# Performance work log

Measured on AMD Instinct MI355X. Metric: run time of the kernel, lower is better.

The kernel has to match this reference:

```python
import jax, jax.numpy as jnp
import numpy as np

N = 100000   # nodes
E = 1600000  # edges
G = 256      # graphs in batch
F_IN = 64
H = 64
C = 10


def setup_inputs() -> dict:
    key = jax.random.key(0)
    ks = jax.random.split(key, 16)
    x = jax.random.normal(ks[0], (N, F_IN), dtype=jnp.float32)
    edge_index = jax.random.randint(ks[1], (2, E), 0, N, dtype=jnp.int32)
    batch = jnp.sort(jax.random.randint(ks[2], (N,), 0, G, dtype=jnp.int32))
    def lin(k, i, o):
        return jax.random.normal(k, (i, o), dtype=jnp.float32) / np.sqrt(i).astype(np.float32)
    return {
        'x': x, 'edge_index': edge_index, 'batch': batch,
        'W1': lin(ks[3], F_IN, H), 'b1': jnp.zeros((H,), jnp.float32),
        'W2': lin(ks[4], H, H),    'b2': jnp.zeros((H,), jnp.float32),
        'W3': lin(ks[5], H, H),    'b3': jnp.zeros((H,), jnp.float32),
        'fc1_w': lin(ks[6], 3 * H, H),      'fc1_b': jnp.zeros((H,), jnp.float32),
        'fc2_w': lin(ks[7], H, H // 2),     'fc2_b': jnp.zeros((H // 2,), jnp.float32),
        'fc3_w': lin(ks[8], H // 2, C),     'fc3_b': jnp.zeros((C,), jnp.float32),
    }


def _gcn_layer(h_in, W, b, src, dst, deg_inv_sqrt):
    # GCNConv: h = X W ; out = D^-1/2 (A + I) D^-1/2 h + b ; then ReLU
    h = h_in @ W
    norm = deg_inv_sqrt[src] * deg_inv_sqrt[dst]            # [E]
    agg = jax.ops.segment_sum(h[src] * norm[:, None], dst, num_segments=N)
    agg = agg + h * (deg_inv_sqrt * deg_inv_sqrt)[:, None]  # self-loop term
    return jax.nn.relu(agg + b)


def _pool(h, batch):
    # concat(mean, max, add) pooling by graph id
    s = jax.ops.segment_sum(h, batch, num_segments=G)
    cnt = jax.ops.segment_sum(jnp.ones((h.shape[0], 1), h.dtype), batch, num_segments=G)
    mean = s / jnp.maximum(cnt, 1.0)
    mx = jnp.maximum(jax.ops.segment_max(h, batch, num_segments=G), 0.0)  # h >= 0 post-ReLU
    return jnp.concatenate([mean, mx, s], axis=1)  # [G, 3H]


def reference(x, edge_index, batch, W1, b1, W2, b2, W3, b3,
              fc1_w, fc1_b, fc2_w, fc2_b, fc3_w, fc3_b):
    src, dst = edge_index[0], edge_index[1]
    # degree including self loop (edge weight 1)
    deg = jax.ops.segment_sum(jnp.ones((E,), x.dtype), dst, num_segments=N) + 1.0
    dis = jax.lax.rsqrt(deg)

    h1 = _gcn_layer(x, W1, b1, src, dst, dis)
    p1 = _pool(h1, batch)
    h2 = _gcn_layer(h1, W2, b2, src, dst, dis)
    p2 = _pool(h2, batch)
    h3 = _gcn_layer(h2, W3, b3, src, dst, dis)
    p3 = _pool(h3, batch)

    z = p1 + p2 + p3                              # [G, 3H]
    z = jax.nn.relu(z @ fc1_w + fc1_b)            # dropout inactive (eval)
    z = jax.nn.relu(z @ fc2_w + fc2_b)
    return jax.nn.log_softmax(z @ fc3_w + fc3_b, axis=-1)
```

## Files before the change

### kernel.cpp

```cpp
#include <hip/hip_runtime.h>
#include <cmath>

typedef unsigned int uint;
typedef __attribute__((ext_vector_type(8))) short short8;
typedef __attribute__((ext_vector_type(4))) float f32x4;
typedef __attribute__((ext_vector_type(4))) int i32x4;

__device__ inline float bflo(uint u) { return __uint_as_float(u << 16); }
__device__ inline float bfhi(uint u) { return __uint_as_float(u & 0xffff0000u); }
__device__ inline ushort bf1(float a) {
  uint ua = __float_as_uint(a);
  return (ushort)((ua + 0x7fffu + ((ua >> 16) & 1u)) >> 16);
}
__device__ inline uint bfpack(float a, float b) {
  uint ua = __float_as_uint(a), ub = __float_as_uint(b);
  uint ra = (ua + 0x7fffu + ((ua >> 16) & 1u)) >> 16;
  uint rb = (ub + 0x7fffu + ((ub >> 16) & 1u)) >> 16;
  return ra | (rb << 16);
}

#define SLOT_CAP 48
#define FILL_CHUNK 4096
#define BSHIFT 8
#define NPB 256
#define MAXB 512
#define BCAP 5120
#define PSPLIT 4

__global__ __launch_bounds__(256) void part_k(const int* __restrict__ src, const int* __restrict__ dst,
                                              int* __restrict__ bcnt, long long* __restrict__ buckets,
                                              int E, int nb) {
  __shared__ int lcnt[MAXB], lbase[MAXB];
  int t = threadIdx.x;
  for (int i = t; i < nb; i += 256) lcnt[i] = 0;
  __syncthreads();
  int base = blockIdx.x * FILL_CHUNK;
  int d[16];
  #pragma unroll
  for (int i = 0; i < 16; ++i) {
    int e = base + t + i * 256;
    d[i] = (e < E) ? __builtin_nontemporal_load(dst + e) : -1;
    if (d[i] >= 0) atomicAdd(&lcnt[d[i] >> BSHIFT], 1);
  }
  __syncthreads();
  for (int i = t; i < nb; i += 256) { lbase[i] = atomicAdd(&bcnt[i], lcnt[i]); lcnt[i] = 0; }
  __syncthreads();
  #pragma unroll
  for (int i = 0; i < 16; ++i) {
    if (d[i] >= 0) {
      int e = base + t + i * 256;
      int r = d[i] >> BSHIFT;
      int rank = atomicAdd(&lcnt[r], 1);
      long long s = (long long)__builtin_nontemporal_load(src + e);
      long long packed = (s << 32) | (unsigned int)d[i];
      buckets[(size_t)r * BCAP + lbase[r] + rank] = packed;
    }
  }
}

__global__ __launch_bounds__(256) void fillB_k(const long long* __restrict__ buckets,
                                               const int* __restrict__ bcnt,
                                               int* __restrict__ cursor, int* __restrict__ csr,
                                               float* __restrict__ dis,
                                               int nb, int N) {
  __shared__ int lcnt[NPB];
  __shared__ int rows[NPB][SLOT_CAP];
  int r = blockIdx.x;
  int t = threadIdx.x;
  if (t < NPB) lcnt[t] = 0;
  i32x4* rinit = (i32x4*)&rows[0][0];
  for (int i = t; i < NPB * SLOT_CAP / 4; i += 256) rinit[i] = (i32x4){N, N, N, N};
  __syncthreads();
  int n = bcnt[r];
  const long long* bk = buckets + (size_t)r * BCAP;
  for (int i = t; i < n; i += 256) {
    long long e = __builtin_nontemporal_load(&bk[i]);
    int dl = (int)(e & (NPB - 1));
    int s = (int)(e >> 32);
    int pos = atomicAdd(&lcnt[dl], 1);
    if (pos < SLOT_CAP) rows[dl][pos] = s;
  }
  __syncthreads();
  int base_node = r << BSHIFT;
  int nodes_here = N - base_node; if (nodes_here > NPB) nodes_here = NPB;
  if (nodes_here <= 0) return;
  int total4 = nodes_here * (SLOT_CAP / 4);
  i32x4* dstp = (i32x4*)(csr + (size_t)base_node * SLOT_CAP);
  const i32x4* srcp = (const i32x4*)&rows[0][0];
  for (int i = t; i < total4; i += 256) dstp[i] = srcp[i];
  for (int i = t; i < nodes_here; i += 256) {
    int c = lcnt[i];
    cursor[base_node + i] = c;
    dis[base_node + i] = rsqrtf((float)c + 1.0f);
  }
}

__global__ __launch_bounds__(256) void bounds_k(const int* __restrict__ batch, int* __restrict__ gstart,
                                                int n, int G) {
  int i = blockIdx.x * 256 + threadIdx.x;
  if (i >= n) return;
  int b = batch[i];
  int prev = (i == 0) ? -1 : batch[i - 1];
  for (int g = prev + 1; g <= b; ++g) gstart[g] = i;
  if (i == n - 1) { for (int g = b + 1; g <= G; ++g) gstart[g] = n; }
}

__global__ __launch_bounds__(256) void xcast_k(const float* __restrict__ X, ushort* __restrict__ Y, int total4) {
  int i = blockIdx.x * 256 + threadIdx.x;
  if (i >= total4) return;
  float4 v = ((const float4*)X)[i];
  ((uint2*)Y)[i] = make_uint2(bfpack(v.x, v.y), bfpack(v.z, v.w));
}

__global__ __launch_bounds__(256) void wt3_k(const float* __restrict__ W1, const float* __restrict__ W2,
                                             const float* __restrict__ W3,
                                             ushort* __restrict__ T1, ushort* __restrict__ T2,
                                             ushort* __restrict__ T3) {
  int b = blockIdx.x >> 4;
  int i = (blockIdx.x & 15) * 256 + threadIdx.x;
  const float* W = (b == 0) ? W1 : (b == 1) ? W2 : W3;
  ushort* T = (b == 0) ? T1 : (b == 1) ? T2 : T3;
  int c = i >> 6, k = i & 63;
  T[i] = bf1(W[k * 64 + c]);
}

__global__ __launch_bounds__(256) void gemm_mfma_k(const ushort* __restrict__ X,
                                                   const ushort* __restrict__ WT,
                                                   const float* __restrict__ dis,
                                                   ushort* __restrict__ Y, int n) {
  int t = threadIdx.x;
  int wv = t >> 6, lane = t & 63;
  int m = lane & 15, quad = lane >> 4;
  int row = blockIdx.x * 64 + wv * 16 + m;
  int rclamp = (row < n) ? row : 0;
  const short8* arow = (const short8*)(X + (size_t)rclamp * 64);
  short8 a0 = arow[quad];
  short8 a1 = arow[quad + 4];
  f32x4 acc[4];
  #pragma unroll
  for (int ct = 0; ct < 4; ++ct) {
    const short8* wrow = (const short8*)(WT + (size_t)(ct * 16 + m) * 64);
    short8 b0 = wrow[quad];
    short8 b1 = wrow[quad + 4];
    f32x4 a = {0.f, 0.f, 0.f, 0.f};
    a = __builtin_amdgcn_mfma_f32_16x16x32_bf16(a0, b0, a, 0, 0, 0);
    a = __builtin_amdgcn_mfma_f32_16x16x32_bf16(a1, b1, a, 0, 0, 0);
    acc[ct] = a;
  }
  int orow = blockIdx.x * 64 + wv * 16 + quad * 4;
  #pragma unroll
  for (int reg = 0; reg < 4; ++reg) {
    int r = orow + reg;
    if (r < n) {
      float ds = dis[r];
      #pragma unroll
      for (int ct = 0; ct < 4; ++ct)
        Y[(size_t)r * 64 + ct * 16 + m] = bf1(acc[ct][reg] * ds);
    }
  }
}

__global__ __launch_bounds__(256) void agg_k(const ushort* __restrict__ Hs,
                                             const int* __restrict__ csr,
                                             const int* __restrict__ cnt,
                                             const float* __restrict__ dis,
                                             const float* __restrict__ bias,
                                             ushort* __restrict__ Hout, int n) {
  int wv = __builtin_amdgcn_readfirstlane((int)(threadIdx.x >> 6));
  int lane = threadIdx.x & 63;
  int node = blockIdx.x * 4 + wv;
  if (node >= n) return;
  float dn = dis[node];
  int deg = __builtin_nontemporal_load(cnt + node);
  if (deg > SLOT_CAP) deg = SLOT_CAP;
  const i32x4* rp = (const i32x4*)(csr + (size_t)node * SLOT_CAP);
  float acc = bflo((uint)Hs[(size_t)node * 64 + lane]);

  i32x4 r0 = __builtin_nontemporal_load(rp + 0);
  i32x4 r1 = __builtin_nontemporal_load(rp + 1);
  i32x4 r2 = __builtin_nontemporal_load(rp + 2);
  i32x4 r3 = __builtin_nontemporal_load(rp + 3);
  i32x4 r4 = __builtin_nontemporal_load(rp + 4);
  i32x4 r5 = __builtin_nontemporal_load(rp + 5);
  i32x4 r6 = __builtin_nontemporal_load(rp + 6);
  i32x4 r7 = __builtin_nontemporal_load(rp + 7);
  int sa[32] = {r0.x, r0.y, r0.z, r0.w, r1.x, r1.y, r1.z, r1.w,
                r2.x, r2.y, r2.z, r2.w, r3.x, r3.y, r3.z, r3.w,
                r4.x, r4.y, r4.z, r4.w, r5.x, r5.y, r5.z, r5.w,
                r6.x, r6.y, r6.z, r6.w, r7.x, r7.y, r7.z, r7.w};
  float ha[32];
  #pragma unroll
  for (int i = 0; i < 32; ++i) ha[i] = bflo((uint)Hs[(size_t)sa[i] * 64 + lane]);
  #pragma unroll
  for (int i = 0; i < 32; ++i) acc += ha[i];

  if (deg > 32) {
    i32x4 r8  = __builtin_nontemporal_load(rp + 8);
    i32x4 r9  = __builtin_nontemporal_load(rp + 9);
    i32x4 r10 = __builtin_nontemporal_load(rp + 10);
    i32x4 r11 = __builtin_nontemporal_load(rp + 11);
    int sb[16] = {r8.x, r8.y, r8.z, r8.w, r9.x, r9.y, r9.z, r9.w,
                  r10.x, r10.y, r10.z, r10.w, r11.x, r11.y, r11.z, r11.w};
    float hb[16];
    #pragma unroll
    for (int i = 0; i < 16; ++i) hb[i] = bflo((uint)Hs[(size_t)sb[i] * 64 + lane]);
    #pragma unroll
    for (int i = 0; i < 16; ++i) acc += hb[i];
  }

  float v = fmaxf(fmaf(dn, acc, bias[lane]), 0.f);
  Hout[(size_t)node * 64 + lane] = bf1(v);
}

__global__ __launch_bounds__(256) void pool_k(const ushort* __restrict__ H, const int* __restrict__ gstart,
                                              float* __restrict__ zsum, uint* __restrict__ zmax) {
  int g = blockIdx.x / PSPLIT;
  int q = blockIdx.x % PSPLIT;
  int t = threadIdx.x;
  int lane = t & 63, w = t >> 6;
  int slot = lane >> 3, fl = lane & 7;
  int i0 = gstart[g], i1 = gstart[g + 1];
  float s[8], m[8];
  #pragma unroll
  for (int j = 0; j < 8; ++j) { s[j] = 0.f; m[j] = 0.f; }
  for (int i = i0 + q * 32 + w * 8 + slot; i < i1; i += 32 * PSPLIT) {
    uint4 v = ((const uint4*)(H + (size_t)i * 64))[fl];
    float f[8] = { bflo(v.x), bfhi(v.x), bflo(v.y), bfhi(v.y),
                   bflo(v.z), bfhi(v.z), bflo(v.w), bfhi(v.w) };
    #pragma unroll
    for (int j = 0; j < 8; ++j) { s[j] += f[j]; m[j] = fmaxf(m[j], f[j]); }
  }
  #pragma unroll
  for (int msk = 8; msk <= 32; msk <<= 1) {
    #pragma unroll
    for (int j = 0; j < 8; ++j) {
      s[j] += __shfl_xor(s[j], msk, 64);
      m[j] = fmaxf(m[j], __shfl_xor(m[j], msk, 64));
    }
  }
  __shared__ float ss[4][64], sm[4][64];
  if (slot == 0) {
    #pragma unroll
    for (int j = 0; j < 8; ++j) { ss[w][fl * 8 + j] = s[j]; sm[w][fl * 8 + j] = m[j]; }
  }
  __syncthreads();
  if (t < 64) {
    float S = (ss[0][t] + ss[1][t]) + (ss[2][t] + ss[3][t]);
    float M = fmaxf(fmaxf(sm[0][t], sm[1][t]), fmaxf(sm[2][t], sm[3][t]));
    atomicAdd(&zsum[g * 64 + t], S);
    atomicMax(&zmax[g * 64 + t], __float_as_uint(M));
  }
}

__global__ __launch_bounds__(64) void mlp_k(const float* __restrict__ zsum,
                                            const uint* __restrict__ zmax, int G64,
                                            const int* __restrict__ gstart,
                                            const float* __restrict__ fc1w, const float* __restrict__ fc1b,
                                            const float* __restrict__ fc2w, const float* __restrict__ fc2b,
                                            const float* __restrict__ fc3w, const float* __restrict__ fc3b,
                                            float* __restrict__ out) {
  int g = blockIdx.x; int t = threadIdx.x;
  __shared__ float zr[192], a1[64], a2[32], a3[10];
  float S = zsum[g * 64 + t];
  float M = __uint_as_float(zmax[g * 64 + t])
          + __uint_as_float(zmax[G64 + g * 64 + t])
          + __uint_as_float(zmax[2 * G64 + g * 64 + t]);
  float cntf = (float)(gstart[g + 1] - gstart[g]);
  zr[t]       = (cntf > 0.f) ? S / cntf : 0.f;
  zr[64 + t]  = M;
  zr[128 + t] = S;
  __syncthreads();
  float acc = fc1b[t];
  for (int k = 0; k < 192; ++k) acc += zr[k] * fc1w[k * 64 + t];
  a1[t] = fmaxf(acc, 0.f);
  __syncthreads();
  if (t < 32) {
    float a = fc2b[t];
    #pragma unroll
    for (int k = 0; k < 64; ++k) a += a1[k] * fc2w[k * 32 + t];
    a2[t] = fmaxf(a, 0.f);
  }
  __syncthreads();
  if (t < 10) {
    float a = fc3b[t];
    #pragma unroll
    for (int k = 0; k < 32; ++k) a += a2[k] * fc3w[k * 10 + t];
    a3[t] = a;
  }
  __syncthreads();
  if (t == 0) {
    float mx = a3[0];
    for (int i = 1; i < 10; ++i) mx = fmaxf(mx, a3[i]);
    float sum = 0.f;
    for (int i = 0; i < 10; ++i) sum += expf(a3[i] - mx);
    float lse = mx + logf(sum);
    for (int i = 0; i < 10; ++i) out[g * 10 + i] = a3[i] - lse;
  }
}

extern "C" void kernel_launch(void* const* d_in, const int* in_sizes, int n_in,
                              void* d_out, int out_size, void* d_ws, size_t ws_size,
                              hipStream_t stream) {
  const float* x    = (const float*)d_in[0];
  const int*   ei   = (const int*)  d_in[1];
  const int*   batch= (const int*)  d_in[2];
  const float* W1   = (const float*)d_in[3];
  const float* b1   = (const float*)d_in[4];
  const float* W2   = (const float*)d_in[5];
  const float* b2   = (const float*)d_in[6];
  const float* W3   = (const float*)d_in[7];
  const float* b3   = (const float*)d_in[8];
  const float* fc1w = (const float*)d_in[9];
  const float* fc1b = (const float*)d_in[10];
  const float* fc2w = (const float*)d_in[11];
  const float* fc2b = (const float*)d_in[12];
  const float* fc3w = (const float*)d_in[13];
  const float* fc3b = (const float*)d_in[14];
  float* out = (float*)d_out;

  const int N = in_sizes[0] / 64;
  const int E = in_sizes[1] / 2;
  const int G = out_size / 10;
  const int* src = ei;
  const int* dst = ei + E;
  const int nb = (N + NPB - 1) >> BSHIFT;

  char* p = (char*)d_ws;
  auto alloc = [&](size_t bytes) -> void* {
    void* r = (void*)p; p += (bytes + 255) & ~(size_t)255; return r;
  };
  int*       cursor  = (int*)      alloc((size_t)N * 4);
  int*       bcnt    = (int*)      alloc(MAXB * 4);
  float*     dis     = (float*)    alloc((size_t)N * 4);
  int*       gstart  = (int*)      alloc((size_t)(G + 1) * 4);
  int*       csr     = (int*)      alloc((size_t)(nb * NPB) * SLOT_CAP * 4);
  long long* buckets = (long long*)alloc((size_t)nb * BCAP * 8);
  ushort*    xbf     = (ushort*)   alloc((size_t)N * 64 * 2);
  ushort*    wt1     = (ushort*)   alloc(4096 * 2);
  ushort*    wt2     = (ushort*)   alloc(4096 * 2);
  ushort*    wt3     = (ushort*)   alloc(4096 * 2);
  ushort*    hlin    = (ushort*)   alloc((size_t)(N + 1) * 64 * 2);
  ushort*    hA      = (ushort*)   alloc((size_t)N * 64 * 2);
  float*     zsum    = (float*)    alloc((size_t)G * 64 * 4);
  uint*      zmax    = (uint*)     alloc((size_t)3 * G * 64 * 4);
  (void)ws_size; (void)n_in;

  (void)hipMemsetAsync(bcnt, 0, MAXB * 4, stream);
  (void)hipMemsetAsync(zsum, 0, (size_t)G * 64 * 4, stream);
  (void)hipMemsetAsync(zmax, 0, (size_t)3 * G * 64 * 4, stream);
  (void)hipMemsetAsync(hlin + (size_t)N * 64, 0, 64 * 2, stream);

  int chunks = (E + FILL_CHUNK - 1) / FILL_CHUNK;
  part_k<<<chunks, 256, 0, stream>>>(src, dst, bcnt, buckets, E, nb);
  fillB_k<<<nb, 256, 0, stream>>>(buckets, bcnt, cursor, csr, dis, nb, N);
  bounds_k<<<(N + 255) / 256, 256, 0, stream>>>(batch, gstart, N, G);
  xcast_k<<<(N * 16 + 255) / 256, 256, 0, stream>>>(x, xbf, N * 16);
  wt3_k<<<48, 256, 0, stream>>>(W1, W2, W3, wt1, wt2, wt3);

  int gb = (N + 63) / 64;
  int ab = (N + 3) / 4;
  int G64 = G * 64;
  gemm_mfma_k<<<gb, 256, 0, stream>>>(xbf, wt1, dis, hlin, N);
  agg_k<<<ab, 256, 0, stream>>>(hlin, csr, cursor, dis, b1, hA, N);
  pool_k<<<G * PSPLIT, 256, 0, stream>>>(hA, gstart, zsum, zmax + 0 * G64);
  gemm_mfma_k<<<gb, 256, 0, stream>>>(hA, wt2, dis, hlin, N);
  agg_k<<<ab, 256, 0, stream>>>(hlin, csr, cursor, dis, b2, hA, N);
  pool_k<<<G * PSPLIT, 256, 0, stream>>>(hA, gstart, zsum, zmax + 1 * G64);
  gemm_mfma_k<<<gb, 256, 0, stream>>>(hA, wt3, dis, hlin, N);
  agg_k<<<ab, 256, 0, stream>>>(hlin, csr, cursor, dis, b3, hA, N);
  pool_k<<<G * PSPLIT, 256, 0, stream>>>(hA, gstart, zsum, zmax + 2 * G64);

  mlp_k<<<G, 64, 0, stream>>>(zsum, zmax, G64, gstart, fc1w, fc1b, fc2w, fc2b, fc3w, fc3b, out);
}
```

Baseline: 321.1 us.

## Fuse setup kernels, pack bucket edges into 32 bits, cast x inside GEMM

Merges the weight transpose, graph-bound computation and all the memsets into one prep kernel, which cuts launch and memset overhead. Bucket entries shrink from 64-bit to 32-bit by packing the source id with the local destination offset, halving partition traffic. This packing assumes source ids fit in 24 bits. The separate x-to-bf16 cast kernel is removed, and the first GEMM now reads fp32 x and converts it in registers.

```diff
diff --git a/kernel.cpp b/kernel.cpp
--- a/kernel.cpp
+++ b/kernel.cpp
@@ -27,8 +27,41 @@
 #define BCAP 5120
 #define PSPLIT 4
 
+__global__ __launch_bounds__(256) void prep_k(const float* __restrict__ W1, const float* __restrict__ W2,
+                                              const float* __restrict__ W3,
+                                              ushort* __restrict__ T1, ushort* __restrict__ T2,
+                                              ushort* __restrict__ T3,
+                                              const int* __restrict__ batch, int* __restrict__ gstart,
+                                              int* __restrict__ bcnt, ushort* __restrict__ hlin,
+                                              float* __restrict__ zpool, int zcount,
+                                              int n, int G, int bnd) {
+  int b = blockIdx.x;
+  int t = threadIdx.x;
+  if (b < 48) {
+    int sel = b >> 4;
+    int i = (b & 15) * 256 + t;
+    const float* W = (sel == 0) ? W1 : (sel == 1) ? W2 : W3;
+    ushort* T = (sel == 0) ? T1 : (sel == 1) ? T2 : T3;
+    int c = i >> 6, k = i & 63;
+    T[i] = bf1(W[k * 64 + c]);
+  } else if (b < 48 + bnd) {
+    int i = (b - 48) * 256 + t;
+    if (i >= n) return;
+    int bb = batch[i];
+    int prev = (i == 0) ? -1 : batch[i - 1];
+    for (int g = prev + 1; g <= bb; ++g) gstart[g] = i;
+    if (i == n - 1) { for (int g = bb + 1; g <= G; ++g) gstart[g] = n; }
+  } else if (b == 48 + bnd) {
+    if (t < 32) ((uint*)(hlin + (size_t)n * 64))[t] = 0u;
+    bcnt[t] = 0; bcnt[t + 256] = 0;
+  } else {
+    int idx = (b - 49 - bnd) * 256 + t;
+    if (idx < zcount) zpool[idx] = 0.f;
+  }
+}
+
 __global__ __launch_bounds__(256) void part_k(const int* __restrict__ src, const int* __restrict__ dst,
-                                              int* __restrict__ bcnt, long long* __restrict__ buckets,
+                                              int* __restrict__ bcnt, uint* __restrict__ buckets,
                                               int E, int nb) {
   __shared__ int lcnt[MAXB], lbase[MAXB];
   int t = threadIdx.x;
@@ -51,14 +84,14 @@
       int e = base + t + i * 256;
       int r = d[i] >> BSHIFT;
       int rank = atomicAdd(&lcnt[r], 1);
-      long long s = (long long)__builtin_nontemporal_load(src + e);
-      long long packed = (s << 32) | (unsigned int)d[i];
+      uint s = (uint)__builtin_nontemporal_load(src + e);
+      uint packed = (s << 8) | (uint)(d[i] & (NPB - 1));
       buckets[(size_t)r * BCAP + lbase[r] + rank] = packed;
     }
   }
 }
 
-__global__ __launch_bounds__(256) void fillB_k(const long long* __restrict__ buckets,
+__global__ __launch_bounds__(256) void fillB_k(const uint* __restrict__ buckets,
                                                const int* __restrict__ bcnt,
                                                int* __restrict__ cursor, int* __restrict__ csr,
                                                float* __restrict__ dis,
@@ -72,11 +105,11 @@
   for (int i = t; i < NPB * SLOT_CAP / 4; i += 256) rinit[i] = (i32x4){N, N, N, N};
   __syncthreads();
   int n = bcnt[r];
-  const long long* bk = buckets + (size_t)r * BCAP;
+  const uint* bk = buckets + (size_t)r * BCAP;
   for (int i = t; i < n; i += 256) {
-    long long e = __builtin_nontemporal_load(&bk[i]);
+    uint e = __builtin_nontemporal_load(&bk[i]);
     int dl = (int)(e & (NPB - 1));
-    int s = (int)(e >> 32);
+    int s = (int)(e >> 8);
     int pos = atomicAdd(&lcnt[dl], 1);
     if (pos < SLOT_CAP) rows[dl][pos] = s;
   }
@@ -95,36 +128,8 @@
   }
 }
 
-__global__ __launch_bounds__(256) void bounds_k(const int* __restrict__ batch, int* __restrict__ gstart,
-                                                int n, int G) {
-  int i = blockIdx.x * 256 + threadIdx.x;
-  if (i >= n) return;
-  int b = batch[i];
-  int prev = (i == 0) ? -1 : batch[i - 1];
-  for (int g = prev + 1; g <= b; ++g) gstart[g] = i;
-  if (i == n - 1) { for (int g = b + 1; g <= G; ++g) gstart[g] = n; }
-}
-
-__global__ __launch_bounds__(256) void xcast_k(const float* __restrict__ X, ushort* __restrict__ Y, int total4) {
-  int i = blockIdx.x * 256 + threadIdx.x;
-  if (i >= total4) return;
-  float4 v = ((const float4*)X)[i];
-  ((uint2*)Y)[i] = make_uint2(bfpack(v.x, v.y), bfpack(v.z, v.w));
-}
-
-__global__ __launch_bounds__(256) void wt3_k(const float* __restrict__ W1, const float* __restrict__ W2,
-                                             const float* __restrict__ W3,
-                                             ushort* __restrict__ T1, ushort* __restrict__ T2,
-                                             ushort* __restrict__ T3) {
-  int b = blockIdx.x >> 4;
-  int i = (blockIdx.x & 15) * 256 + threadIdx.x;
-  const float* W = (b == 0) ? W1 : (b == 1) ? W2 : W3;
-  ushort* T = (b == 0) ? T1 : (b == 1) ? T2 : T3;
-  int c = i >> 6, k = i & 63;
-  T[i] = bf1(W[k * 64 + c]);
-}
-
 __global__ __launch_bounds__(256) void gemm_mfma_k(const ushort* __restrict__ X,
+                                                   const float* __restrict__ Xf,
                                                    const ushort* __restrict__ WT,
                                                    const float* __restrict__ dis,
                                                    ushort* __restrict__ Y, int n) {
@@ -133,9 +138,22 @@
   int m = lane & 15, quad = lane >> 4;
   int row = blockIdx.x * 64 + wv * 16 + m;
   int rclamp = (row < n) ? row : 0;
-  const short8* arow = (const short8*)(X + (size_t)rclamp * 64);
-  short8 a0 = arow[quad];
-  short8 a1 = arow[quad + 4];
+  short8 a0, a1;
+  if (Xf) {
+    const float4* af = (const float4*)(Xf + (size_t)rclamp * 64);
+    float4 v0 = af[quad * 2],     v1 = af[quad * 2 + 1];
+    float4 v2 = af[quad * 2 + 8], v3 = af[quad * 2 + 9];
+    union { uint u[4]; short8 s; } c0, c1;
+    c0.u[0] = bfpack(v0.x, v0.y); c0.u[1] = bfpack(v0.z, v0.w);
+    c0.u[2] = bfpack(v1.x, v1.y); c0.u[3] = bfpack(v1.z, v1.w);
+    c1.u[0] = bfpack(v2.x, v2.y); c1.u[1] = bfpack(v2.z, v2.w);
+    c1.u[2] = bfpack(v3.x, v3.y); c1.u[3] = bfpack(v3.z, v3.w);
+    a0 = c0.s; a1 = c1.s;
+  } else {
+    const short8* arow = (const short8*)(X + (size_t)rclamp * 64);
+    a0 = arow[quad];
+    a1 = arow[quad + 4];
+  }
   f32x4 acc[4];
   #pragma unroll
   for (int ct = 0; ct < 4; ++ct) {
@@ -334,39 +352,36 @@
   float*     dis     = (float*)    alloc((size_t)N * 4);
   int*       gstart  = (int*)      alloc((size_t)(G + 1) * 4);
   int*       csr     = (int*)      alloc((size_t)(nb * NPB) * SLOT_CAP * 4);
-  long long* buckets = (long long*)alloc((size_t)nb * BCAP * 8);
-  ushort*    xbf     = (ushort*)   alloc((size_t)N * 64 * 2);
+  uint*      buckets = (uint*)     alloc((size_t)nb * BCAP * 4);
   ushort*    wt1     = (ushort*)   alloc(4096 * 2);
   ushort*    wt2     = (ushort*)   alloc(4096 * 2);
   ushort*    wt3     = (ushort*)   alloc(4096 * 2);
   ushort*    hlin    = (ushort*)   alloc((size_t)(N + 1) * 64 * 2);
   ushort*    hA      = (ushort*)   alloc((size_t)N * 64 * 2);
-  float*     zsum    = (float*)    alloc((size_t)G * 64 * 4);
-  uint*      zmax    = (uint*)     alloc((size_t)3 * G * 64 * 4);
+  float*     zpool   = (float*)    alloc((size_t)4 * G * 64 * 4);
+  float*     zsum    = zpool;
+  uint*      zmax    = (uint*)(zpool + (size_t)G * 64);
   (void)ws_size; (void)n_in;
 
-  (void)hipMemsetAsync(bcnt, 0, MAXB * 4, stream);
-  (void)hipMemsetAsync(zsum, 0, (size_t)G * 64 * 4, stream);
-  (void)hipMemsetAsync(zmax, 0, (size_t)3 * G * 64 * 4, stream);
-  (void)hipMemsetAsync(hlin + (size_t)N * 64, 0, 64 * 2, stream);
-
+  int G64 = G * 64;
+  int bnd = (N + 255) >> 8;
+  int zcount = 4 * G64;
+  int prep_grid = 48 + bnd + 1 + (zcount + 255) / 256;
+  prep_k<<<prep_grid, 256, 0, stream>>>(W1, W2, W3, wt1, wt2, wt3, batch, gstart,
+                                        bcnt, hlin, zpool, zcount, N, G, bnd);
   int chunks = (E + FILL_CHUNK - 1) / FILL_CHUNK;
   part_k<<<chunks, 256, 0, stream>>>(src, dst, bcnt, buckets, E, nb);
   fillB_k<<<nb, 256, 0, stream>>>(buckets, bcnt, cursor, csr, dis, nb, N);
-  bounds_k<<<(N + 255) / 256, 256, 0, stream>>>(batch, gstart, N, G);
-  xcast_k<<<(N * 16 + 255) / 256, 256, 0, stream>>>(x, xbf, N * 16);
-  wt3_k<<<48, 256, 0, stream>>>(W1, W2, W3, wt1, wt2, wt3);
 
   int gb = (N + 63) / 64;
   int ab = (N + 3) / 4;
-  int G64 = G * 64;
-  gemm_mfma_k<<<gb, 256, 0, stream>>>(xbf, wt1, dis, hlin, N);
+  gemm_mfma_k<<<gb, 256, 0, stream>>>(nullptr, x, wt1, dis, hlin, N);
   agg_k<<<ab, 256, 0, stream>>>(hlin, csr, cursor, dis, b1, hA, N);
   pool_k<<<G * PSPLIT, 256, 0, stream>>>(hA, gstart, zsum, zmax + 0 * G64);
-  gemm_mfma_k<<<gb, 256, 0, stream>>>(hA, wt2, dis, hlin, N);
+  gemm_mfma_k<<<gb, 256, 0, stream>>>(hA, nullptr, wt2, dis, hlin, N);
   agg_k<<<ab, 256, 0, stream>>>(hlin, csr, cursor, dis, b2, hA, N);
   pool_k<<<G * PSPLIT, 256, 0, stream>>>(hA, gstart, zsum, zmax + 1 * G64);
-  gemm_mfma_k<<<gb, 256, 0, stream>>>(hA, wt3, dis, hlin, N);
+  gemm_mfma_k<<<gb, 256, 0, stream>>>(hA, nullptr, wt3, dis, hlin, N);
   agg_k<<<ab, 256, 0, stream>>>(hlin, csr, cursor, dis, b3, hA, N);
   pool_k<<<G * PSPLIT, 256, 0, stream>>>(hA, gstart, zsum, zmax + 2 * G64);
 
```

Measured after the change: 302.8 us. 5.7% less time.
